# Kernel tuning notes

Hardware: AMD Instinct MI355X
Metric: run time of the kernel (lower is better)

## Reference

```python
import jax, jax.numpy as jnp
import numpy as np

P, H_OUT, D, NX = 32, 1, 256, 16
S_A = -0.1

def layernorm(x, g, b, eps=1e-5):
    mu = jnp.mean(x, axis=-1, keepdims=True)
    var = jnp.var(x, axis=-1, keepdims=True)
    return (x - mu) * jax.lax.rsqrt(var + eps) * g + b

def setup_inputs() -> dict:
    key = jax.random.key(0)
    ks = jax.random.split(key, 16)
    B, L = 8, 2048
    y = jax.random.normal(ks[0], (B, L, P), jnp.float32)
    Win = jax.random.normal(ks[1], (P, D), jnp.float32) / np.sqrt(P)
    bin_ = jnp.zeros((D,), jnp.float32)
    ng = jnp.ones((D,), jnp.float32); nb = jnp.zeros((D,), jnp.float32)
    # A = -10*rand + s_A, with A[:,0] = s_A (fix first state of each channel)
    A = -10.0 * jax.random.uniform(ks[2], (D, NX), jnp.float32) + S_A
    A = A.at[:, 0].set(S_A)
    W_B = jax.random.normal(ks[3], (NX, D), jnp.float32)
    W_C = jax.random.normal(ks[4], (NX, D), jnp.float32)
    q_delta = jax.random.normal(ks[5], (D,), jnp.float32)
    p_delta = jax.random.normal(ks[6], (1,), jnp.float32)
    nfg = jnp.ones((D,), jnp.float32); nfb = jnp.zeros((D,), jnp.float32)
    W1 = jax.random.normal(ks[7], (D, D), jnp.float32) / np.sqrt(D)
    b1 = jnp.zeros((D,), jnp.float32)
    W2 = jax.random.normal(ks[8], (D, H_OUT * P), jnp.float32) / np.sqrt(D)
    b2 = jnp.zeros((H_OUT * P,), jnp.float32)
    return {"y": y, "Win": Win, "bin_": bin_, "ng": ng, "nb": nb, "A": A,
            "W_B": W_B, "W_C": W_C, "q_delta": q_delta, "p_delta": p_delta,
            "nfg": nfg, "nfb": nfb, "W1": W1, "b1": b1, "W2": W2, "b2": b2}

def selective_scan(u, delta, A, Bm, Cm):
    # u: (B,L,D), delta: (B,L), A: (D,NX), Bm/Cm: (B,L,NX)
    dA = jnp.exp(delta[..., None, None] * A)                      # (B,L,D,NX)
    dBu = delta[..., None, None] * Bm[:, :, None, :] * u[..., None]  # (B,L,D,NX)
    x0 = jnp.zeros((u.shape[0], u.shape[2], A.shape[1]), u.dtype)
    def step(x, inp):
        dA_t, dBu_t, C_t = inp
        x = dA_t * x + dBu_t                                      # (B,D,NX)
        y_t = jnp.einsum('bdn,bn->bd', x, C_t)
        return x, y_t
    _, ys = jax.lax.scan(step, x0, (dA.transpose(1, 0, 2, 3),
                                    dBu.transpose(1, 0, 2, 3),
                                    Cm.transpose(1, 0, 2)))
    return ys.transpose(1, 0, 2)                                  # (B,L,D)

def reference(y, Win, bin_, ng, nb, A, W_B, W_C, q_delta, p_delta,
              nfg, nfb, W1, b1, W2, b2):
    B, L, _ = y.shape
    h = y @ Win + bin_                                            # (B,L,D)
    hn = layernorm(h, ng, nb)
    delta = jax.nn.softplus(p_delta[0] + jnp.einsum('bld,d->bl', hn, q_delta))
    Bm = jnp.einsum('nd,bld->bln', W_B, hn)
    Cm = jnp.einsum('nd,bld->bln', W_C, hn)
    upd = selective_scan(hn, delta, A, Bm, Cm)
    h = h + upd
    h = layernorm(h, nfg, nfb)
    out = jax.nn.gelu(h @ W1 + b1, approximate=False) @ W2 + b2
    return out.reshape(B, L, H_OUT, P)
```

## Files before the change

### kernel.cpp

```cpp
#include <hip/hip_runtime.h>
#include <math.h>

#define D 256
#define NX 16
#define L 2048
#define NBATCH 8
#define NTOK (NBATCH * L)
#define CL 32
#define NCH (L / CL)
#define LOG2E 1.44269504088896340736f

typedef float f32x4 __attribute__((ext_vector_type(4)));
typedef short bf16x8 __attribute__((ext_vector_type(8)));

__device__ __forceinline__ unsigned short f2bf(float x) {
  unsigned u = __float_as_uint(x);
  u = u + 0x7fffu + ((u >> 16) & 1u);
  return (unsigned short)(u >> 16);
}
__device__ __forceinline__ float bf2f(unsigned short h) {
  return __uint_as_float(((unsigned)h) << 16);
}

__global__ __launch_bounds__(256) void k0_prep(const float* __restrict__ A,
                                               const float* __restrict__ WB,
                                               const float* __restrict__ WC,
                                               const float* __restrict__ Win,
                                               const float* __restrict__ W1,
                                               const float* __restrict__ W2,
                                               float* __restrict__ At,
                                               unsigned short* __restrict__ W1fh,
                                               unsigned short* __restrict__ W1fl,
                                               unsigned short* __restrict__ W2fh,
                                               unsigned short* __restrict__ W2fl,
                                               unsigned short* __restrict__ Winfh,
                                               unsigned short* __restrict__ Winfl,
                                               unsigned short* __restrict__ Wbcfh,
                                               unsigned short* __restrict__ Wbcfl) {
  int i = blockIdx.x * 256 + threadIdx.x;
  if (i < 4096) {
    int d = i >> 4, n = i & 15;
    At[n * D + d] = A[i] * LOG2E;
  } else if (i < 12288) {
    int e = i - 4096;
    int j = e & 7, l = (e >> 3) & 63, tt = e >> 9;
    int k = ((l >> 4) << 3) + j;
    int n = tt * 16 + (l & 15);
    float x = Win[k * 256 + n];
    unsigned short h = f2bf(x);
    Winfh[e] = h;
    Winfl[e] = f2bf(x - bf2f(h));
  } else if (i < 20480) {
    int e = i - 12288;
    int j = e & 7, l = (e >> 3) & 63, q = e >> 9;
    int s = q >> 1, tt = q & 1;
    int k = s * 32 + ((l >> 4) << 3) + j;
    int n = tt * 16 + (l & 15);
    float x = (n < 16) ? WB[n * 256 + k] : WC[(n - 16) * 256 + k];
    unsigned short h = f2bf(x);
    Wbcfh[e] = h;
    Wbcfl[e] = f2bf(x - bf2f(h));
  } else if (i < 86016) {
    int e = i - 20480;
    int j = e & 7, l = (e >> 3) & 63, tt = (e >> 9) & 15, s = e >> 13;
    int k = s * 32 + ((l >> 4) << 3) + j;
    int n = tt * 16 + (l & 15);
    float x = W1[k * 256 + n];
    unsigned short h = f2bf(x);
    W1fh[e] = h;
    W1fl[e] = f2bf(x - bf2f(h));
  } else {
    int e = i - 86016;
    int j = e & 7, l = (e >> 3) & 63, tt = (e >> 9) & 1, s = e >> 10;
    int k = s * 32 + ((l >> 4) << 3) + j;
    int n = tt * 16 + (l & 15);
    float x = W2[k * 32 + n];
    unsigned short h = f2bf(x);
    W2fh[e] = h;
    W2fl[e] = f2bf(x - bf2f(h));
  }
}

__global__ __launch_bounds__(512, 4) void k1a_front_scan(
    const float* __restrict__ y, const float* __restrict__ bin_,
    const float* __restrict__ ng, const float* __restrict__ nb,
    const float* __restrict__ qd, const float* __restrict__ pd,
    const float* __restrict__ At,
    const unsigned short* __restrict__ Winfh,
    const unsigned short* __restrict__ Winfl,
    const unsigned short* __restrict__ Wbcfh,
    const unsigned short* __restrict__ Wbcfl,
    float* __restrict__ hn, float* __restrict__ delta,
    float* __restrict__ Bm, float* __restrict__ Cm,
    float* __restrict__ muv, float* __restrict__ irsv,
    float* __restrict__ EX, float* __restrict__ T) {
  __shared__ float sy[32][36];
  __shared__ float sh[32][260];
  __shared__ float sB[32][NX];
  __shared__ float sred[32][16];
  __shared__ float sdelta[32];
  __shared__ float smu[32];
  __shared__ float srstd[32];
  __shared__ __align__(16) unsigned short sChA_h[32 * 256];
  __shared__ __align__(16) unsigned short sChA_l[32 * 256];
  int t = threadIdx.x;
  int l = t & 63;
  int w = t >> 6;
  int tok0 = blockIdx.x * 32;
  if (t < 256) {
    int row = t >> 3, c4 = t & 7;
    *(float4*)&sy[row][c4 * 4] = ((const float4*)(y + (size_t)tok0 * 32))[t];
  }
  __syncthreads();
  f32x4 acc[2][2];
  {
    bf16x8 yah[2], yal[2];
    int k0 = (l >> 4) << 3;
    #pragma unroll
    for (int m = 0; m < 2; ++m) {
      int row = m * 16 + (l & 15);
      float4 f0 = *(float4*)&sy[row][k0];
      float4 f1 = *(float4*)&sy[row][k0 + 4];
      float v0 = f0.x, v1 = f0.y, v2 = f0.z, v3 = f0.w;
      float v4 = f1.x, v5 = f1.y, v6 = f1.z, v7 = f1.w;
      unsigned short h0 = f2bf(v0), h1 = f2bf(v1), h2 = f2bf(v2), h3 = f2bf(v3);
      unsigned short h4 = f2bf(v4), h5 = f2bf(v5), h6 = f2bf(v6), h7 = f2bf(v7);
      yah[m][0] = (short)h0; yah[m][1] = (short)h1; yah[m][2] = (short)h2; yah[m][3] = (short)h3;
      yah[m][4] = (short)h4; yah[m][5] = (short)h5; yah[m][6] = (short)h6; yah[m][7] = (short)h7;
      yal[m][0] = (short)f2bf(v0 - bf2f(h0)); yal[m][1] = (short)f2bf(v1 - bf2f(h1));
      yal[m][2] = (short)f2bf(v2 - bf2f(h2)); yal[m][3] = (short)f2bf(v3 - bf2f(h3));
      yal[m][4] = (short)f2bf(v4 - bf2f(h4)); yal[m][5] = (short)f2bf(v5 - bf2f(h5));
      yal[m][6] = (short)f2bf(v6 - bf2f(h6)); yal[m][7] = (short)f2bf(v7 - bf2f(h7));
    }
    const bf16x8* Bh = (const bf16x8*)Winfh;
    const bf16x8* Bl = (const bf16x8*)Winfl;
    #pragma unroll
    for (int n = 0; n < 2; ++n) {
      int tt = w * 2 + n;
      bf16x8 bh = Bh[tt * 64 + l];
      bf16x8 bl = Bl[tt * 64 + l];
      #pragma unroll
      for (int m = 0; m < 2; ++m) {
        f32x4 a = {0.f, 0.f, 0.f, 0.f};
        a = __builtin_amdgcn_mfma_f32_16x16x32_bf16(yah[m], bh, a, 0, 0, 0);
        a = __builtin_amdgcn_mfma_f32_16x16x32_bf16(yal[m], bh, a, 0, 0, 0);
        a = __builtin_amdgcn_mfma_f32_16x16x32_bf16(yah[m], bl, a, 0, 0, 0);
        a = __builtin_amdgcn_mfma_f32_16x16x32_bf16(yal[m], bl, a, 0, 0, 0);
        acc[m][n] = a;
      }
    }
  }
  int c0 = w * 32 + (l & 15), c1 = c0 + 16;
  {
    float b0 = bin_[c0], b1v = bin_[c1];
    #pragma unroll
    for (int m = 0; m < 2; ++m)
      #pragma unroll
      for (int r = 0; r < 4; ++r) { acc[m][0][r] += b0; acc[m][1][r] += b1v; }
  }
  {
    #pragma unroll
    for (int m = 0; m < 2; ++m)
      #pragma unroll
      for (int r = 0; r < 4; ++r) {
        float a0 = acc[m][0][r], a1 = acc[m][1][r];
        float s1 = a0 + a1;
        float s2 = a0 * a0 + a1 * a1;
        #pragma unroll
        for (int off = 1; off < 16; off <<= 1) {
          s1 += __shfl_xor(s1, off);
          s2 += __shfl_xor(s2, off);
        }
        if ((l & 15) == 0) {
          int tok = m * 16 + ((l >> 4) << 2) + r;
          sred[tok][w * 2] = s1;
          sred[tok][w * 2 + 1] = s2;
        }
      }
  }
  __syncthreads();
  if (t < 32) {
    float s1 = 0.f, s2 = 0.f;
    #pragma unroll
    for (int q = 0; q < 8; ++q) { s1 += sred[t][q * 2]; s2 += sred[t][q * 2 + 1]; }
    float mu = s1 * (1.f / D);
    float var = s2 * (1.f / D) - mu * mu;
    float rstd = rsqrtf(var + 1e-5f);
    smu[t] = mu;
    srstd[t] = rstd;
    muv[tok0 + t] = mu;
    irsv[tok0 + t] = sqrtf(var + 1e-5f);
  }
  __syncthreads();
  {
    float g0 = ng[c0], g1 = ng[c1];
    float nb0 = nb[c0], nb1 = nb[c1];
    float q0 = qd[c0], q1 = qd[c1];
    float ddv[2][4];
    #pragma unroll
    for (int m = 0; m < 2; ++m)
      #pragma unroll
      for (int r = 0; r < 4; ++r) {
        int tok = m * 16 + ((l >> 4) << 2) + r;
        float mu = smu[tok], rstd = srstd[tok];
        float h0 = (acc[m][0][r] - mu) * rstd * g0 + nb0;
        float h1 = (acc[m][1][r] - mu) * rstd * g1 + nb1;
        sh[tok][c0] = h0;
        sh[tok][c1] = h1;
        float dx = h0 * q0 + h1 * q1;
        #pragma unroll
        for (int off = 1; off < 16; off <<= 1) dx += __shfl_xor(dx, off);
        ddv[m][r] = dx;
      }
    if ((l & 15) == 0) {
      #pragma unroll
      for (int m = 0; m < 2; ++m)
        #pragma unroll
        for (int r = 0; r < 4; ++r)
          sred[m * 16 + ((l >> 4) << 2) + r][w] = ddv[m][r];
    }
  }
  __syncthreads();
  if (t < 32) {
    float dsum = 0.f;
    #pragma unroll
    for (int q = 0; q < 8; ++q) dsum += sred[t][q];
    float xx = pd[0] + dsum;
    float dv = (xx > 20.f) ? xx : log1pf(expf(xx));
    delta[tok0 + t] = dv;
    sdelta[t] = dv;
    float tv = dv;
    #pragma unroll
    for (int off = 1; off < 32; off <<= 1) tv += __shfl_xor(tv, off);
    if (t == 0) T[blockIdx.x] = tv;
  }
  {
    int row = t & 31;
    int cq = (t >> 5) * 16;
    float4 f0 = *(float4*)&sh[row][cq];
    float4 f1 = *(float4*)&sh[row][cq + 4];
    float4 f2 = *(float4*)&sh[row][cq + 8];
    float4 f3 = *(float4*)&sh[row][cq + 12];
    float vv[16] = {f0.x, f0.y, f0.z, f0.w, f1.x, f1.y, f1.z, f1.w,
                    f2.x, f2.y, f2.z, f2.w, f3.x, f3.y, f3.z, f3.w};
    unsigned hw[8], lw[8];
    #pragma unroll
    for (int p = 0; p < 8; ++p) {
      unsigned short ha = f2bf(vv[2 * p]), hb = f2bf(vv[2 * p + 1]);
      unsigned short la = f2bf(vv[2 * p] - bf2f(ha));
      unsigned short lb = f2bf(vv[2 * p + 1] - bf2f(hb));
      hw[p] = (unsigned)ha | ((unsigned)hb << 16);
      lw[p] = (unsigned)la | ((unsigned)lb << 16);
    }
    unsigned base = (unsigned)row * 512;
    #pragma unroll
    for (int g = 0; g < 2; ++g) {
      unsigned off = ((unsigned)(cq * 2 + g * 16)) ^ ((unsigned)(row & 7) << 4);
      uint4 hv4 = {hw[g * 4], hw[g * 4 + 1], hw[g * 4 + 2], hw[g * 4 + 3]};
      uint4 lv4 = {lw[g * 4], lw[g * 4 + 1], lw[g * 4 + 2], lw[g * 4 + 3]};
      *(uint4*)((char*)sChA_h + base + off) = hv4;
      *(uint4*)((char*)sChA_l + base + off) = lv4;
    }
  }
  __syncthreads();
  if (w < 4) {
    int mw = w & 1, nw = w >> 1;
    int row = mw * 16 + (l & 15);
    unsigned abase = (unsigned)row * 512;
    const bf16x8* B2h = (const bf16x8*)Wbcfh;
    const bf16x8* B2l = (const bf16x8*)Wbcfl;
    f32x4 acc2 = {0.f, 0.f, 0.f, 0.f};
    #pragma unroll
    for (int s = 0; s < 8; ++s) {
      unsigned off = ((unsigned)(s * 64 + ((l >> 4) << 4))) ^ ((unsigned)(row & 7) << 4);
      bf16x8 ah = *(const bf16x8*)((const char*)sChA_h + abase + off);
      bf16x8 al = *(const bf16x8*)((const char*)sChA_l + abase + off);
      int bi = (s * 2 + nw) * 64 + l;
      bf16x8 bh = B2h[bi];
      bf16x8 bl = B2l[bi];
      acc2 = __builtin_amdgcn_mfma_f32_16x16x32_bf16(ah, bh, acc2, 0, 0, 0);
      acc2 = __builtin_amdgcn_mfma_f32_16x16x32_bf16(al, bh, acc2, 0, 0, 0);
      acc2 = __builtin_amdgcn_mfma_f32_16x16x32_bf16(ah, bl, acc2, 0, 0, 0);
      acc2 = __builtin_amdgcn_mfma_f32_16x16x32_bf16(al, bl, acc2, 0, 0, 0);
    }
    int tokr = mw * 16 + ((l >> 4) << 2);
    int colc = l & 15;
    if (nw == 0) {
      #pragma unroll
      for (int r = 0; r < 4; ++r) {
        Bm[(size_t)(tok0 + tokr + r) * NX + colc] = acc2[r];
        sB[tokr + r][colc] = acc2[r];
      }
    } else {
      #pragma unroll
      for (int r = 0; r < 4; ++r)
        Cm[(size_t)(tok0 + tokr + r) * NX + colc] = acc2[r];
    }
  } else {
    float4* dst = (float4*)(hn + (size_t)tok0 * D);
    for (int i = t - 256; i < 2048; i += 256) {
      int row = i >> 6, c4 = i & 63;
      dst[i] = *(float4*)&sh[row][c4 * 4];
    }
  }
  __syncthreads();
  {
    int half = t >> 8;
    int d = t & 255;
    float a8[8], x8[8];
    #pragma unroll
    for (int n = 0; n < 8; ++n) {
      a8[n] = At[(half * 8 + n) * D + d];
      x8[n] = 0.f;
    }
    for (int lo = 0; lo < CL; ++lo) {
      float dlt = sdelta[lo];
      float du = dlt * sh[lo][d];
      #pragma unroll
      for (int n = 0; n < 8; ++n)
        x8[n] = fmaf(exp2f(dlt * a8[n]), x8[n], du * sB[lo][half * 8 + n]);
    }
    size_t exbase = (size_t)blockIdx.x * (NX * D) + d;
    #pragma unroll
    for (int n = 0; n < 8; ++n) EX[exbase + (half * 8 + n) * D] = x8[n];
  }
}

__global__ __launch_bounds__(64) void k2b_chunkscan(
    const float* __restrict__ At, const float* __restrict__ T,
    float* __restrict__ EX) {
  __shared__ float sT[NCH];
  int b = blockIdx.x >> 6;
  int rem = ((blockIdx.x & 63) << 6) | threadIdx.x;
  sT[threadIdx.x] = T[b * NCH + threadIdx.x];
  __syncthreads();
  float A2 = At[rem];
  size_t base = ((size_t)b << 18) + rem;
  float eq[8];
  #pragma unroll
  for (int j = 0; j < 8; ++j) eq[j] = EX[base + ((size_t)j << 12)];
  float x = 0.f;
  #pragma unroll 8
  for (int c = 0; c < NCH; ++c) {
    float e = eq[c & 7];
    if (c + 8 < NCH) eq[c & 7] = EX[base + ((size_t)(c + 8) << 12)];
    EX[base + ((size_t)c << 12)] = x;
    x = fmaf(exp2f(sT[c] * A2), x, e);
  }
}

__device__ __forceinline__ float gelu_exact(float x) {
  return 0.5f * x * (1.f + erff(x * 0.70710678118654752440f));
}

__global__ __launch_bounds__(256) void k2cd_scan_mlp(
    const float* __restrict__ hn, const float* __restrict__ delta,
    const float* __restrict__ Bm, const float* __restrict__ Cm,
    const float* __restrict__ At, const float* __restrict__ EX,
    const float* __restrict__ muv, const float* __restrict__ irsv,
    const float* __restrict__ ng, const float* __restrict__ nb,
    const float* __restrict__ nfg, const float* __restrict__ nfb,
    const unsigned short* __restrict__ W1fh, const unsigned short* __restrict__ W1fl,
    const unsigned short* __restrict__ W2fh, const unsigned short* __restrict__ W2fl,
    const float* __restrict__ b1, const float* __restrict__ b2,
    float* __restrict__ out) {
  __shared__ float s_az[32 * 260];
  __shared__ __align__(16) unsigned short sAh[32 * 256];
  __shared__ __align__(16) unsigned short sAl[32 * 256];
  __shared__ float sB[32][NX];
  __shared__ float sC[32][NX];
  __shared__ float sdelta[32];
  __shared__ float smu[32];
  __shared__ float sirs[32];
  int t = threadIdx.x;
  int tok0 = blockIdx.x * 32;
  size_t tokbase = (size_t)tok0;
  if (t < 32) {
    sdelta[t] = delta[tokbase + t];
    smu[t] = muv[tokbase + t];
    sirs[t] = irsv[tokbase + t];
  }
  for (int i = t; i < 32 * NX; i += 256) {
    ((float*)sB)[i] = Bm[tokbase * NX + i];
    ((float*)sC)[i] = Cm[tokbase * NX + i];
  }
  float a16[16], x16[16];
  size_t exbase = (size_t)blockIdx.x * (NX * D) + t;
  #pragma unroll
  for (int n = 0; n < 16; ++n) {
    a16[n] = At[n * D + t];
    x16[n] = EX[exbase + n * D];
  }
  float nb_d = nb[t];
  float invg = 1.0f / ng[t];
  __syncthreads();
  for (int lo = 0; lo < CL; ++lo) {
    float hv = hn[(tokbase + lo) * D + t];
    float dlt = sdelta[lo];
    float du = dlt * hv;
    float p = 0.f;
    #pragma unroll
    for (int n = 0; n < 16; ++n) {
      x16[n] = fmaf(exp2f(dlt * a16[n]), x16[n], du * sB[lo][n]);
      p = fmaf(x16[n], sC[lo][n], p);
    }
    float h = fmaf((hv - nb_d) * invg, sirs[lo], smu[lo]);
    s_az[lo * 260 + t] = h + p;
  }
  __syncthreads();
  int dcol = t & 63, jrow = t >> 6;
  int d4 = dcol * 4, j8 = jrow * 8;
  {
    float4 g4 = ((const float4*)nfg)[dcol];
    float4 b4 = ((const float4*)nfb)[dcol];
    for (int jj = 0; jj < 8; ++jj) {
      int lo = j8 + jj;
      float4 v = *(float4*)&s_az[lo * 260 + d4];
      float s1 = v.x + v.y + v.z + v.w;
      float s2 = v.x * v.x + v.y * v.y + v.z * v.z + v.w * v.w;
      #pragma unroll
      for (int off = 1; off < 64; off <<= 1) {
        s1 += __shfl_xor(s1, off);
        s2 += __shfl_xor(s2, off);
      }
      float mu2 = s1 * (1.f / D);
      float var2 = s2 * (1.f / D) - mu2 * mu2;
      float rstd2 = rsqrtf(var2 + 1e-5f);
      float4 o;
      o.x = (v.x - mu2) * rstd2 * g4.x + b4.x;
      o.y = (v.y - mu2) * rstd2 * g4.y + b4.y;
      o.z = (v.z - mu2) * rstd2 * g4.z + b4.z;
      o.w = (v.w - mu2) * rstd2 * g4.w + b4.w;
      unsigned short h0 = f2bf(o.x), h1 = f2bf(o.y), h2 = f2bf(o.z), h3 = f2bf(o.w);
      unsigned short q0 = f2bf(o.x - bf2f(h0));
      unsigned short q1 = f2bf(o.y - bf2f(h1));
      unsigned short q2 = f2bf(o.z - bf2f(h2));
      unsigned short q3 = f2bf(o.w - bf2f(h3));
      unsigned off16 = ((unsigned)(d4 * 2)) ^ ((unsigned)(lo & 7) << 4);
      uint2 hv2, lv2;
      hv2.x = (unsigned)h0 | ((unsigned)h1 << 16);
      hv2.y = (unsigned)h2 | ((unsigned)h3 << 16);
      lv2.x = (unsigned)q0 | ((unsigned)q1 << 16);
      lv2.y = (unsigned)q2 | ((unsigned)q3 << 16);
      *(uint2*)((char*)sAh + lo * 512 + off16) = hv2;
      *(uint2*)((char*)sAl + lo * 512 + off16) = lv2;
    }
  }
  __syncthreads();
  int l = t & 63, w = t >> 6;
  const bf16x8* B1h = (const bf16x8*)W1fh;
  const bf16x8* B1l = (const bf16x8*)W1fl;
  f32x4 acc[2][4];
  #pragma unroll
  for (int m = 0; m < 2; ++m)
    #pragma unroll
    for (int n = 0; n < 4; ++n) {
      f32x4 z4 = {0.f, 0.f, 0.f, 0.f};
      acc[m][n] = z4;
    }
  #pragma unroll 2
  for (int s = 0; s < 8; ++s) {
    bf16x8 ah[2], al[2];
    #pragma unroll
    for (int m = 0; m < 2; ++m) {
      int row = m * 16 + (l & 15);
      unsigned off16 = ((unsigned)(s * 64 + ((l >> 4) << 4))) ^ ((unsigned)(row & 7) << 4);
      ah[m] = *(const bf16x8*)((const char*)sAh + row * 512 + off16);
      al[m] = *(const bf16x8*)((const char*)sAl + row * 512 + off16);
    }
    #pragma unroll
    for (int n = 0; n < 4; ++n) {
      int bi = (s * 16 + w * 4 + n) * 64 + l;
      bf16x8 bh = B1h[bi];
      bf16x8 bl = B1l[bi];
      #pragma unroll
      for (int m = 0; m < 2; ++m) {
        acc[m][n] = __builtin_amdgcn_mfma_f32_16x16x32_bf16(ah[m], bh, acc[m][n], 0, 0, 0);
        acc[m][n] = __builtin_amdgcn_mfma_f32_16x16x32_bf16(al[m], bh, acc[m][n], 0, 0, 0);
        acc[m][n] = __builtin_amdgcn_mfma_f32_16x16x32_bf16(ah[m], bl, acc[m][n], 0, 0, 0);
        acc[m][n] = __builtin_amdgcn_mfma_f32_16x16x32_bf16(al[m], bl, acc[m][n], 0, 0, 0);
      }
    }
  }
  __syncthreads();
  #pragma unroll
  for (int n = 0; n < 4; ++n) {
    int colz = w * 64 + n * 16 + (l & 15);
    float b1v = b1[colz];
    #pragma unroll
    for (int m = 0; m < 2; ++m) {
      #pragma unroll
      for (int r = 0; r < 4; ++r) {
        int row = m * 16 + ((l >> 4) << 2) + r;
        float zv = gelu_exact(acc[m][n][r] + b1v);
        unsigned short zh = f2bf(zv);
        unsigned short zl = f2bf(zv - bf2f(zh));
        unsigned off16 = ((unsigned)(colz * 2)) ^ ((unsigned)(row & 7) << 4);
        *(unsigned short*)((char*)sAh + row * 512 + off16) = zh;
        *(unsigned short*)((char*)sAl + row * 512 + off16) = zl;
      }
    }
  }
  __syncthreads();
  int mw = w >> 1, nw = w & 1;
  const bf16x8* B2h = (const bf16x8*)W2fh;
  const bf16x8* B2l = (const bf16x8*)W2fl;
  f32x4 acc2 = {0.f, 0.f, 0.f, 0.f};
  #pragma unroll 2
  for (int s = 0; s < 8; ++s) {
    int row = mw * 16 + (l & 15);
    unsigned off16 = ((unsigned)(s * 64 + ((l >> 4) << 4))) ^ ((unsigned)(row & 7) << 4);
    bf16x8 zh8 = *(const bf16x8*)((const char*)sAh + row * 512 + off16);
    bf16x8 zl8 = *(const bf16x8*)((const char*)sAl + row * 512 + off16);
    int bi = (s * 2 + nw) * 64 + l;
    bf16x8 bh = B2h[bi];
    bf16x8 bl = B2l[bi];
    acc2 = __builtin_amdgcn_mfma_f32_16x16x32_bf16(zh8, bh, acc2, 0, 0, 0);
    acc2 = __builtin_amdgcn_mfma_f32_16x16x32_bf16(zl8, bh, acc2, 0, 0, 0);
    acc2 = __builtin_amdgcn_mfma_f32_16x16x32_bf16(zh8, bl, acc2, 0, 0, 0);
    acc2 = __builtin_amdgcn_mfma_f32_16x16x32_bf16(zl8, bl, acc2, 0, 0, 0);
  }
  int colo = nw * 16 + (l & 15);
  float b2v = b2[colo];
  #pragma unroll
  for (int r = 0; r < 4; ++r) {
    int row = mw * 16 + ((l >> 4) << 2) + r;
    out[(size_t)(tok0 + row) * 32 + colo] = acc2[r] + b2v;
  }
}

extern "C" void kernel_launch(void* const* d_in, const int* in_sizes, int n_in,
                              void* d_out, int out_size, void* d_ws, size_t ws_size,
                              hipStream_t stream) {
  const float* y    = (const float*)d_in[0];
  const float* Win  = (const float*)d_in[1];
  const float* bin_ = (const float*)d_in[2];
  const float* ng   = (const float*)d_in[3];
  const float* nb   = (const float*)d_in[4];
  const float* A    = (const float*)d_in[5];
  const float* WB   = (const float*)d_in[6];
  const float* WC   = (const float*)d_in[7];
  const float* qd   = (const float*)d_in[8];
  const float* pd   = (const float*)d_in[9];
  const float* nfg  = (const float*)d_in[10];
  const float* nfb  = (const float*)d_in[11];
  const float* W1   = (const float*)d_in[12];
  const float* b1   = (const float*)d_in[13];
  const float* W2   = (const float*)d_in[14];
  const float* b2   = (const float*)d_in[15];

  float* ws = (float*)d_ws;
  float* hnbuf = ws;
  float* delta = ws + 4194304;
  float* Bm    = delta + NTOK;
  float* Cm    = Bm + NTOK * NX;
  float* muv   = Cm + NTOK * NX;
  float* irsv  = muv + NTOK;
  float* Tbuf  = irsv + NTOK;
  float* At    = Tbuf + NBATCH * NCH;
  float* EX    = At + D * NX;
  unsigned short* W1fh  = (unsigned short*)(EX + 2097152);
  unsigned short* W1fl  = W1fh + 65536;
  unsigned short* W2fh  = W1fl + 65536;
  unsigned short* W2fl  = W2fh + 8192;
  unsigned short* Winfh = W2fl + 8192;
  unsigned short* Winfl = Winfh + 8192;
  unsigned short* Wbcfh = Winfl + 8192;
  unsigned short* Wbcfl = Wbcfh + 8192;

  k0_prep<<<368, 256, 0, stream>>>(A, WB, WC, Win, W1, W2, At,
                                   W1fh, W1fl, W2fh, W2fl,
                                   Winfh, Winfl, Wbcfh, Wbcfl);
  k1a_front_scan<<<NTOK / 32, 512, 0, stream>>>(y, bin_, ng, nb, qd, pd, At,
                                                Winfh, Winfl, Wbcfh, Wbcfl,
                                                hnbuf, delta, Bm, Cm,
                                                muv, irsv, EX, Tbuf);
  k2b_chunkscan<<<NBATCH * 64, 64, 0, stream>>>(At, Tbuf, EX);
  k2cd_scan_mlp<<<NTOK / 32, 256, 0, stream>>>(hnbuf, delta, Bm, Cm, At, EX,
                                               muv, irsv, ng, nb, nfg, nfb,
                                               W1fh, W1fl, W2fh, W2fl,
                                               b1, b2, (float*)d_out);
}
```

Measured before the change: 182.1 us.

## Fold final layernorm into W1 GEMM epilogue via precomputed column sums

Folds the final layernorm into the first MLP matmul: nfg is pre-multiplied into W1, and per-column sums u1 = nfg·W1 and v1 = nfb·W1 are precomputed in the prep kernel. The GEMM then runs on the un-normalized residual, and the per-row mean and rstd are applied in the epilogue as acc*rstd - mu*rstd*u1 + v1. This removes a shared-memory staging buffer, one normalization pass and one barrier, and adds launch_bounds occupancy hints. The cost is a serial 256-iteration loop per thread in the prep kernel and possible precision loss when mean times u1 is large relative to the result.

```diff
diff --git a/kernel.cpp b/kernel.cpp
--- a/kernel.cpp
+++ b/kernel.cpp
@@ -28,6 +28,8 @@
                                                const float* __restrict__ Win,
                                                const float* __restrict__ W1,
                                                const float* __restrict__ W2,
+                                               const float* __restrict__ nfg,
+                                               const float* __restrict__ nfb,
                                                float* __restrict__ At,
                                                unsigned short* __restrict__ W1fh,
                                                unsigned short* __restrict__ W1fl,
@@ -36,7 +38,9 @@
                                                unsigned short* __restrict__ Winfh,
                                                unsigned short* __restrict__ Winfl,
                                                unsigned short* __restrict__ Wbcfh,
-                                               unsigned short* __restrict__ Wbcfl) {
+                                               unsigned short* __restrict__ Wbcfl,
+                                               float* __restrict__ u1,
+                                               float* __restrict__ v1) {
   int i = blockIdx.x * 256 + threadIdx.x;
   if (i < 4096) {
     int d = i >> 4, n = i & 15;
@@ -65,11 +69,11 @@
     int j = e & 7, l = (e >> 3) & 63, tt = (e >> 9) & 15, s = e >> 13;
     int k = s * 32 + ((l >> 4) << 3) + j;
     int n = tt * 16 + (l & 15);
-    float x = W1[k * 256 + n];
+    float x = W1[k * 256 + n] * nfg[k];
     unsigned short h = f2bf(x);
     W1fh[e] = h;
     W1fl[e] = f2bf(x - bf2f(h));
-  } else {
+  } else if (i < 94208) {
     int e = i - 86016;
     int j = e & 7, l = (e >> 3) & 63, tt = (e >> 9) & 1, s = e >> 10;
     int k = s * 32 + ((l >> 4) << 3) + j;
@@ -78,6 +82,16 @@
     unsigned short h = f2bf(x);
     W2fh[e] = h;
     W2fl[e] = f2bf(x - bf2f(h));
+  } else if (i < 94464) {
+    int c = i - 94208;
+    float s = 0.f;
+    for (int d = 0; d < 256; ++d) s += nfg[d] * W1[d * 256 + c];
+    u1[c] = s;
+  } else if (i < 94720) {
+    int c = i - 94464;
+    float s = 0.f;
+    for (int d = 0; d < 256; ++d) s += nfb[d] * W1[d * 256 + c];
+    v1[c] = s;
   }
 }
 
@@ -121,13 +135,13 @@
       int row = m * 16 + (l & 15);
       float4 f0 = *(float4*)&sy[row][k0];
       float4 f1 = *(float4*)&sy[row][k0 + 4];
-      float v0 = f0.x, v1 = f0.y, v2 = f0.z, v3 = f0.w;
+      float v0 = f0.x, v1_ = f0.y, v2 = f0.z, v3 = f0.w;
       float v4 = f1.x, v5 = f1.y, v6 = f1.z, v7 = f1.w;
-      unsigned short h0 = f2bf(v0), h1 = f2bf(v1), h2 = f2bf(v2), h3 = f2bf(v3);
+      unsigned short h0 = f2bf(v0), h1 = f2bf(v1_), h2 = f2bf(v2), h3 = f2bf(v3);
       unsigned short h4 = f2bf(v4), h5 = f2bf(v5), h6 = f2bf(v6), h7 = f2bf(v7);
       yah[m][0] = (short)h0; yah[m][1] = (short)h1; yah[m][2] = (short)h2; yah[m][3] = (short)h3;
       yah[m][4] = (short)h4; yah[m][5] = (short)h5; yah[m][6] = (short)h6; yah[m][7] = (short)h7;
-      yal[m][0] = (short)f2bf(v0 - bf2f(h0)); yal[m][1] = (short)f2bf(v1 - bf2f(h1));
+      yal[m][0] = (short)f2bf(v0 - bf2f(h0)); yal[m][1] = (short)f2bf(v1_ - bf2f(h1));
       yal[m][2] = (short)f2bf(v2 - bf2f(h2)); yal[m][3] = (short)f2bf(v3 - bf2f(h3));
       yal[m][4] = (short)f2bf(v4 - bf2f(h4)); yal[m][5] = (short)f2bf(v5 - bf2f(h5));
       yal[m][6] = (short)f2bf(v6 - bf2f(h6)); yal[m][7] = (short)f2bf(v7 - bf2f(h7));
@@ -353,32 +367,35 @@
   return 0.5f * x * (1.f + erff(x * 0.70710678118654752440f));
 }
 
-__global__ __launch_bounds__(256) void k2cd_scan_mlp(
+__global__ __launch_bounds__(256, 4) void k2cd_scan_mlp(
     const float* __restrict__ hn, const float* __restrict__ delta,
     const float* __restrict__ Bm, const float* __restrict__ Cm,
     const float* __restrict__ At, const float* __restrict__ EX,
     const float* __restrict__ muv, const float* __restrict__ irsv,
     const float* __restrict__ ng, const float* __restrict__ nb,
-    const float* __restrict__ nfg, const float* __restrict__ nfb,
     const unsigned short* __restrict__ W1fh, const unsigned short* __restrict__ W1fl,
     const unsigned short* __restrict__ W2fh, const unsigned short* __restrict__ W2fl,
+    const float* __restrict__ u1, const float* __restrict__ v1,
     const float* __restrict__ b1, const float* __restrict__ b2,
     float* __restrict__ out) {
-  __shared__ float s_az[32 * 260];
   __shared__ __align__(16) unsigned short sAh[32 * 256];
   __shared__ __align__(16) unsigned short sAl[32 * 256];
   __shared__ float sB[32][NX];
   __shared__ float sC[32][NX];
   __shared__ float sdelta[32];
-  __shared__ float smu[32];
-  __shared__ float sirs[32];
+  __shared__ float smu1[32];
+  __shared__ float sirs1[32];
+  __shared__ float sstat[32][8];
+  __shared__ float srstd2[32];
+  __shared__ float smur2[32];
   int t = threadIdx.x;
+  int l = t & 63, w = t >> 6;
   int tok0 = blockIdx.x * 32;
   size_t tokbase = (size_t)tok0;
   if (t < 32) {
     sdelta[t] = delta[tokbase + t];
-    smu[t] = muv[tokbase + t];
-    sirs[t] = irsv[tokbase + t];
+    smu1[t] = muv[tokbase + t];
+    sirs1[t] = irsv[tokbase + t];
   }
   for (int i = t; i < 32 * NX; i += 256) {
     ((float*)sB)[i] = Bm[tokbase * NX + i];
@@ -404,50 +421,32 @@
       x16[n] = fmaf(exp2f(dlt * a16[n]), x16[n], du * sB[lo][n]);
       p = fmaf(x16[n], sC[lo][n], p);
     }
-    float h = fmaf((hv - nb_d) * invg, sirs[lo], smu[lo]);
-    s_az[lo * 260 + t] = h + p;
-  }
-  __syncthreads();
-  int dcol = t & 63, jrow = t >> 6;
-  int d4 = dcol * 4, j8 = jrow * 8;
-  {
-    float4 g4 = ((const float4*)nfg)[dcol];
-    float4 b4 = ((const float4*)nfb)[dcol];
-    for (int jj = 0; jj < 8; ++jj) {
-      int lo = j8 + jj;
-      float4 v = *(float4*)&s_az[lo * 260 + d4];
-      float s1 = v.x + v.y + v.z + v.w;
-      float s2 = v.x * v.x + v.y * v.y + v.z * v.z + v.w * v.w;
-      #pragma unroll
-      for (int off = 1; off < 64; off <<= 1) {
-        s1 += __shfl_xor(s1, off);
-        s2 += __shfl_xor(s2, off);
-      }
-      float mu2 = s1 * (1.f / D);
-      float var2 = s2 * (1.f / D) - mu2 * mu2;
-      float rstd2 = rsqrtf(var2 + 1e-5f);
-      float4 o;
-      o.x = (v.x - mu2) * rstd2 * g4.x + b4.x;
-      o.y = (v.y - mu2) * rstd2 * g4.y + b4.y;
-      o.z = (v.z - mu2) * rstd2 * g4.z + b4.z;
-      o.w = (v.w - mu2) * rstd2 * g4.w + b4.w;
-      unsigned short h0 = f2bf(o.x), h1 = f2bf(o.y), h2 = f2bf(o.z), h3 = f2bf(o.w);
-      unsigned short q0 = f2bf(o.x - bf2f(h0));
-      unsigned short q1 = f2bf(o.y - bf2f(h1));
-      unsigned short q2 = f2bf(o.z - bf2f(h2));
-      unsigned short q3 = f2bf(o.w - bf2f(h3));
-      unsigned off16 = ((unsigned)(d4 * 2)) ^ ((unsigned)(lo & 7) << 4);
-      uint2 hv2, lv2;
-      hv2.x = (unsigned)h0 | ((unsigned)h1 << 16);
-      hv2.y = (unsigned)h2 | ((unsigned)h3 << 16);
-      lv2.x = (unsigned)q0 | ((unsigned)q1 << 16);
-      lv2.y = (unsigned)q2 | ((unsigned)q3 << 16);
-      *(uint2*)((char*)sAh + lo * 512 + off16) = hv2;
-      *(uint2*)((char*)sAl + lo * 512 + off16) = lv2;
-    }
-  }
-  __syncthreads();
-  int l = t & 63, w = t >> 6;
+    float h = fmaf((hv - nb_d) * invg, sirs1[lo], smu1[lo]);
+    float v = h + p;
+    float s1 = v, s2 = v * v;
+    #pragma unroll
+    for (int off = 1; off < 64; off <<= 1) {
+      s1 += __shfl_xor(s1, off);
+      s2 += __shfl_xor(s2, off);
+    }
+    if (l == 0) { sstat[lo][w * 2] = s1; sstat[lo][w * 2 + 1] = s2; }
+    unsigned short vh = f2bf(v);
+    unsigned short vl = f2bf(v - bf2f(vh));
+    unsigned off16 = ((unsigned)(t * 2)) ^ ((unsigned)((lo & 7) << 4));
+    *(unsigned short*)((char*)sAh + lo * 512 + off16) = vh;
+    *(unsigned short*)((char*)sAl + lo * 512 + off16) = vl;
+  }
+  __syncthreads();
+  if (t < 32) {
+    float s1 = sstat[t][0] + sstat[t][2] + sstat[t][4] + sstat[t][6];
+    float s2 = sstat[t][1] + sstat[t][3] + sstat[t][5] + sstat[t][7];
+    float mu = s1 * (1.f / D);
+    float var = s2 * (1.f / D) - mu * mu;
+    float rstd = rsqrtf(var + 1e-5f);
+    srstd2[t] = rstd;
+    smur2[t] = mu * rstd;
+  }
+  __syncthreads();
   const bf16x8* B1h = (const bf16x8*)W1fh;
   const bf16x8* B1l = (const bf16x8*)W1fl;
   f32x4 acc[2][4];
@@ -486,13 +485,15 @@
   #pragma unroll
   for (int n = 0; n < 4; ++n) {
     int colz = w * 64 + n * 16 + (l & 15);
-    float b1v = b1[colz];
+    float u1c = u1[colz];
+    float v1c = v1[colz] + b1[colz];
     #pragma unroll
     for (int m = 0; m < 2; ++m) {
       #pragma unroll
       for (int r = 0; r < 4; ++r) {
         int row = m * 16 + ((l >> 4) << 2) + r;
-        float zv = gelu_exact(acc[m][n][r] + b1v);
+        float zpre = acc[m][n][r] * srstd2[row] - smur2[row] * u1c + v1c;
+        float zv = gelu_exact(zpre);
         unsigned short zh = f2bf(zv);
         unsigned short zl = f2bf(zv - bf2f(zh));
         unsigned off16 = ((unsigned)(colz * 2)) ^ ((unsigned)(row & 7) << 4);
@@ -567,17 +568,19 @@
   unsigned short* Winfl = Winfh + 8192;
   unsigned short* Wbcfh = Winfl + 8192;
   unsigned short* Wbcfl = Wbcfh + 8192;
-
-  k0_prep<<<368, 256, 0, stream>>>(A, WB, WC, Win, W1, W2, At,
+  float* u1 = (float*)(Wbcfl + 8192);
+  float* v1 = u1 + 256;
+
+  k0_prep<<<370, 256, 0, stream>>>(A, WB, WC, Win, W1, W2, nfg, nfb, At,
                                    W1fh, W1fl, W2fh, W2fl,
-                                   Winfh, Winfl, Wbcfh, Wbcfl);
+                                   Winfh, Winfl, Wbcfh, Wbcfl, u1, v1);
   k1a_front_scan<<<NTOK / 32, 512, 0, stream>>>(y, bin_, ng, nb, qd, pd, At,
                                                 Winfh, Winfl, Wbcfh, Wbcfl,
                                                 hnbuf, delta, Bm, Cm,
                                                 muv, irsv, EX, Tbuf);
   k2b_chunkscan<<<NBATCH * 64, 64, 0, stream>>>(At, Tbuf, EX);
   k2cd_scan_mlp<<<NTOK / 32, 256, 0, stream>>>(hnbuf, delta, Bm, Cm, At, EX,
-                                               muv, irsv, ng, nb, nfg, nfb,
+                                               muv, irsv, ng, nb,
                                                W1fh, W1fl, W2fh, W2fl,
-                                               b1, b2, (float*)d_out);
-}
+                                               u1, v1, b1, b2, (float*)d_out);
+}
```

New measurement: 201.0 us. 1.1x slower.
